# Performance work log

Measured on AMD Instinct MI355X. Metric: run time of the kernel, lower is better.

The kernel has to match this reference:

```python
import jax, jax.numpy as jnp
import numpy as np

D_MODEL = 768
NUM_HEADS = 12
HEAD_DIM = D_MODEL // NUM_HEADS


def setup_inputs() -> dict:
    key = jax.random.key(0)
    ks = jax.random.split(key, 9)
    B, S = 4, 2048
    x = jax.random.normal(ks[0], (B, S, D_MODEL), dtype=jnp.float32)
    y = jax.random.normal(ks[1], (B, S, D_MODEL), dtype=jnp.float32)
    mask = jnp.zeros((1, 1, S, S), dtype=jnp.float32)
    s = 1.0 / np.sqrt(D_MODEL)
    Wq = jax.random.normal(ks[2], (D_MODEL, D_MODEL), dtype=jnp.float32) * s
    bq = jnp.zeros((D_MODEL,), dtype=jnp.float32)
    Wkv = jax.random.normal(ks[3], (2 * D_MODEL, D_MODEL), dtype=jnp.float32) * s
    bkv = jnp.zeros((2 * D_MODEL,), dtype=jnp.float32)
    Wo = jax.random.normal(ks[4], (D_MODEL, D_MODEL), dtype=jnp.float32) * s
    bo = jnp.zeros((D_MODEL,), dtype=jnp.float32)
    return {"x": x, "y": y, "mask": mask, "Wq": Wq, "bq": bq,
            "Wkv": Wkv, "bkv": bkv, "Wo": Wo, "bo": bo}


def reference(x, y, mask, Wq, bq, Wkv, bkv, Wo, bo):
    B, S, _ = x.shape
    H, Dh = NUM_HEADS, HEAD_DIM
    # q = Linear(x); kv = Linear(y)   (torch Linear: x @ W.T + b)
    q = x @ Wq.T + bq                      # [B, S, D]
    kv = y @ Wkv.T + bkv                   # [B, S, 2D]
    q = q.reshape(B, S, H, Dh).transpose(0, 2, 1, 3)          # [B, H, S, Dh]
    kv = kv.reshape(B, S, H, 2 * Dh).transpose(0, 2, 1, 3)    # [B, H, S, 2Dh]
    k, v = kv[..., :Dh], kv[..., Dh:]
    scaled = jnp.einsum('bhqd,bhkd->bhqk', q, k) / jnp.sqrt(jnp.float32(Dh))
    scaled = scaled + mask
    attn = jax.nn.softmax(scaled, axis=-1)                    # [B, H, S, S]
    values = jnp.einsum('bhqk,bhkd->bhqd', attn, v)           # [B, H, S, Dh]
    values = values.transpose(0, 2, 1, 3).reshape(B, S, H * Dh)
    return values @ Wo.T + bo
```

## Files before the change

### kernel.cpp

```cpp
#include <hip/hip_runtime.h>
#include <cstdint>

#define S_LEN 2048
#define BATCH 4
#define NHEADS 12
#define DHEAD 64
#define DMODEL 768
#define SCALE_LOG2E 0.18033688011112042f
#define LOG2E 1.4426950408889634f

typedef unsigned short ushort_t;
typedef __attribute__((ext_vector_type(8))) __bf16 bf16x8;
typedef __attribute__((ext_vector_type(4))) float floatx4;

__device__ __forceinline__ ushort_t f2bf(float f) {
  unsigned u = __builtin_bit_cast(unsigned, f);
  u += 0x7fffu + ((u >> 16) & 1u);
  return (ushort_t)(u >> 16);
}

__device__ __forceinline__ unsigned pk2bf(float a, float b) {
  unsigned ua = __builtin_bit_cast(unsigned, a);
  unsigned ub = __builtin_bit_cast(unsigned, b);
  ua += 0x7fffu + ((ua >> 16) & 1u);
  ub += 0x7fffu + ((ub >> 16) & 1u);
  return __builtin_amdgcn_perm(ub, ua, 0x07060302);
}

__device__ __forceinline__ float fexp2(float x) {
#if __has_builtin(__builtin_amdgcn_exp2f)
  return __builtin_amdgcn_exp2f(x);
#else
  return exp2f(x);
#endif
}

__device__ __forceinline__ void gld16(const void* g, void* s) {
  __builtin_amdgcn_global_load_lds(
      (const __attribute__((address_space(1))) void*)g,
      (__attribute__((address_space(3))) void*)s, 16, 0, 0);
}

__device__ __forceinline__ floatx4 mfma16(bf16x8 a, bf16x8 b, floatx4 c) {
  return __builtin_amdgcn_mfma_f32_16x16x32_bf16(a, b, c, 0, 0, 0);
}

__global__ void init_flag(int* flag) { *flag = 1; }

__global__ void cvt_mask(const float* __restrict__ x, ushort_t* __restrict__ xb,
                         const float* __restrict__ y, ushort_t* __restrict__ yb,
                         const float* __restrict__ wq, ushort_t* __restrict__ wqb,
                         const float* __restrict__ wkv, ushort_t* __restrict__ wkvb,
                         const float* __restrict__ wo, ushort_t* __restrict__ wob,
                         const float* __restrict__ mask, int* __restrict__ flag) {
  int bx = blockIdx.x;
  if (bx >= 14592) {
    int i = (bx - 14592) * 256 + threadIdx.x;
    float4 v = ((const float4*)mask)[i];
    if (v.x != 0.f || v.y != 0.f || v.z != 0.f || v.w != 0.f) *flag = 0;
    return;
  }
  const float* s;
  ushort_t* d;
  int base;
  if (bx < 6144) { s = x; d = xb; base = bx; }
  else if (bx < 12288) { s = y; d = yb; base = bx - 6144; }
  else if (bx < 12864) { s = wq; d = wqb; base = bx - 12288; }
  else if (bx < 14016) { s = wkv; d = wkvb; base = bx - 12864; }
  else { s = wo; d = wob; base = bx - 14016; }
  int i = base * 256 + threadIdx.x;
  float4 v = ((const float4*)s)[i];
  uint2 o;
  o.x = pk2bf(v.x, v.y);
  o.y = pk2bf(v.z, v.w);
  ((uint2*)d)[i] = o;
}

#define GSTAGE(K0, BUF)                                                   \
  {                                                                       \
    gld16(ag + (K0), (char*)As + (BUF)*8192 + (wave << 10));              \
    gld16(ag + (K0) + 64 * K, (char*)As + (BUF)*8192 + (wave << 10) + 4096); \
    gld16(bg + (K0), (char*)Bs + (BUF)*8192 + (wave << 10));              \
    gld16(bg + (K0) + 64 * K, (char*)Bs + (BUF)*8192 + (wave << 10) + 4096); \
  }

__global__ __launch_bounds__(256, 3) void gemm_qkv(
    const ushort_t* __restrict__ xb, const ushort_t* __restrict__ wqb,
    const float* __restrict__ bq, ushort_t* __restrict__ Qh,
    const ushort_t* __restrict__ yb, const ushort_t* __restrict__ wkvb,
    const float* __restrict__ bkv, ushort_t* __restrict__ Kh,
    ushort_t* __restrict__ Vt) {
  __shared__ __align__(16) ushort_t As[2][128 * 32];
  __shared__ __align__(16) ushort_t Bs[2][128 * 32];
  const int tid = threadIdx.x;
  const int wave = tid >> 6, lane = tid & 63;
  const int wm = wave >> 1, wn = wave & 1;
  const bool isQ = blockIdx.x < 6;
  const int bn = (isQ ? blockIdx.x : blockIdx.x - 6) * 128;
  const int bm = blockIdx.y * 128;
  const ushort_t* A = isQ ? xb : yb;
  const ushort_t* W = isQ ? wqb : wkvb;
  const float* bias = isQ ? bq : bkv;
  const int K = DMODEL;
  const int fr = lane & 15, fq = lane >> 4;

  const int rT = tid >> 2;
  const int cT = ((tid & 3) ^ (rT & 3)) << 3;
  const ushort_t* ag = A + (size_t)(bm + rT) * K + cT;
  const ushort_t* bg = W + (size_t)(bn + rT) * K + cT;

  floatx4 acc[4][4] = {};
  GSTAGE(0, 0);
  __syncthreads();
  for (int k0 = 0; k0 < K; k0 += 32) {
    const int cur = (k0 >> 5) & 1;
    if (k0 + 32 < K) GSTAGE(k0 + 32, cur ^ 1);
    const ushort_t* Ac = As[cur];
    const ushort_t* Bc = Bs[cur];
    bf16x8 af[4], bf[4];
#pragma unroll
    for (int i = 0; i < 4; i++)
      af[i] = *(const bf16x8*)(Ac + (wm * 64 + i * 16 + fr) * 32 + ((fq ^ (fr & 3)) << 3));
#pragma unroll
    for (int j = 0; j < 4; j++)
      bf[j] = *(const bf16x8*)(Bc + (wn * 64 + j * 16 + fr) * 32 + ((fq ^ (fr & 3)) << 3));
#pragma unroll
    for (int i = 0; i < 4; i++)
#pragma unroll
      for (int j = 0; j < 4; j++)
        acc[i][j] = mfma16(af[i], bf[j], acc[i][j]);
    __syncthreads();
  }

#pragma unroll
  for (int i = 0; i < 4; i++) {
#pragma unroll
    for (int j = 0; j < 4; j++) {
#pragma unroll
      for (int r = 0; r < 4; r++) {
        int m = bm + wm * 64 + i * 16 + fq * 4 + r;
        int n = bn + wn * 64 + j * 16 + fr;
        float v = acc[i][j][r] + bias[n];
        int b = m >> 11, s = m & 2047;
        if (isQ) {
          int h = n >> 6, d = n & 63;
          Qh[(((size_t)b * NHEADS + h) * S_LEN + s) * DHEAD + d] = f2bf(v * SCALE_LOG2E);
        } else {
          int h = n >> 7, jj = n & 127;
          if (jj < 64) {
            Kh[(((size_t)b * NHEADS + h) * S_LEN + s) * DHEAD + jj] = f2bf(v);
          } else {
            int sp = (s & ~63) | ((s & 15) << 2) | ((s >> 4) & 3);
            Vt[(((size_t)b * NHEADS + h) * DHEAD + (jj - 64)) * S_LEN + sp] = f2bf(v);
          }
        }
      }
    }
  }
}

__global__ __launch_bounds__(256, 3) void gemm_out(
    const ushort_t* __restrict__ A, const ushort_t* __restrict__ W,
    const float* __restrict__ bias, float* __restrict__ o32) {
  __shared__ __align__(16) ushort_t As[2][128 * 32];
  __shared__ __align__(16) ushort_t Bs[2][128 * 32];
  const int tid = threadIdx.x;
  const int wave = tid >> 6, lane = tid & 63;
  const int wm = wave >> 1, wn = wave & 1;
  const int bm = blockIdx.y * 128, bn = blockIdx.x * 128;
  const int K = DMODEL;
  const int fr = lane & 15, fq = lane >> 4;

  const int rT = tid >> 2;
  const int cT = ((tid & 3) ^ (rT & 3)) << 3;
  const ushort_t* ag = A + (size_t)(bm + rT) * K + cT;
  const ushort_t* bg = W + (size_t)(bn + rT) * K + cT;

  floatx4 acc[4][4] = {};
  GSTAGE(0, 0);
  __syncthreads();
  for (int k0 = 0; k0 < K; k0 += 32) {
    const int cur = (k0 >> 5) & 1;
    if (k0 + 32 < K) GSTAGE(k0 + 32, cur ^ 1);
    const ushort_t* Ac = As[cur];
    const ushort_t* Bc = Bs[cur];
    bf16x8 af[4], bf[4];
#pragma unroll
    for (int i = 0; i < 4; i++)
      af[i] = *(const bf16x8*)(Ac + (wm * 64 + i * 16 + fr) * 32 + ((fq ^ (fr & 3)) << 3));
#pragma unroll
    for (int j = 0; j < 4; j++)
      bf[j] = *(const bf16x8*)(Bc + (wn * 64 + j * 16 + fr) * 32 + ((fq ^ (fr & 3)) << 3));
#pragma unroll
    for (int i = 0; i < 4; i++)
#pragma unroll
      for (int j = 0; j < 4; j++)
        acc[i][j] = mfma16(af[i], bf[j], acc[i][j]);
    __syncthreads();
  }

#pragma unroll
  for (int i = 0; i < 4; i++)
#pragma unroll
    for (int j = 0; j < 4; j++)
#pragma unroll
      for (int r = 0; r < 4; r++) {
        int m = bm + wm * 64 + i * 16 + fq * 4 + r;
        int n = bn + wn * 64 + j * 16 + fr;
        o32[(size_t)m * DMODEL + n] = acc[i][j][r] + bias[n];
      }
}

__global__ __launch_bounds__(256, 3) void flash_attn(
    const ushort_t* __restrict__ Qh, const ushort_t* __restrict__ Kh,
    const ushort_t* __restrict__ Vt, const float* __restrict__ mask,
    const int* __restrict__ mask_is_zero, ushort_t* __restrict__ Oh) {
  __shared__ __align__(16) ushort_t Ks[2][64 * 64];
  __shared__ __align__(16) ushort_t Vs[2][64 * 64];
  __shared__ __align__(16) ushort_t Ps[4][32 * 64];
  const int qt = blockIdx.x, bh = blockIdx.y;
  const int b = bh / NHEADS, h = bh % NHEADS;
  const int tid = threadIdx.x, w = tid >> 6, lane = tid & 63;
  const int li = lane & 15, lg = lane >> 4, sx = li & 7;
  const bool use_mask = (*mask_is_zero == 0);

  const int q0 = qt * 128 + w * 32;
  const ushort_t* qg = Qh + ((size_t)bh * S_LEN + q0) * DHEAD;
  bf16x8 qf[2][2];
#pragma unroll
  for (int m = 0; m < 2; m++)
#pragma unroll
    for (int kk = 0; kk < 2; kk++)
      qf[m][kk] = *(const bf16x8*)(qg + (m * 16 + li) * 64 + kk * 32 + lg * 8);

  const int srow = lane >> 3;
  const int schk = (lane & 7) ^ srow;
  const ushort_t* kg = Kh + (size_t)bh * S_LEN * DHEAD;
  const ushort_t* vg = Vt + (size_t)bh * DHEAD * S_LEN;

  float m_i[2][4], l_p[2][4];
  floatx4 o_acc[2][4] = {};
#pragma unroll
  for (int m = 0; m < 2; m++)
#pragma unroll
    for (int r = 0; r < 4; r++) { m_i[m][r] = -1e30f; l_p[m][r] = 0.f; }

#define STAGE(KT, BUF)                                                            \
  {                                                                               \
    const ushort_t* k0_ = kg + (size_t)((KT)*64 + w * 16 + srow) * 64 + schk * 8; \
    gld16(k0_, (char*)Ks + (BUF)*8192 + w * 2048);                                \
    gld16(k0_ + 8 * 64, (char*)Ks + (BUF)*8192 + w * 2048 + 1024);                \
    const ushort_t* v0_ = vg + (size_t)(w * 16 + srow) * 2048 + (KT)*64 + schk * 8; \
    gld16(v0_, (char*)Vs + (BUF)*8192 + w * 2048);                                \
    gld16(v0_ + 8 * 2048, (char*)Vs + (BUF)*8192 + w * 2048 + 1024);              \
  }

  STAGE(0, 0);
  __syncthreads();

  for (int kt = 0; kt < S_LEN / 64; kt++) {
    const int cur = kt & 1;
    if (kt < S_LEN / 64 - 1) STAGE(kt + 1, cur ^ 1);
    const ushort_t* Kc = Ks[cur];
    const ushort_t* Vc = Vs[cur];

    floatx4 sc[2][4];
#pragma unroll
    for (int c = 0; c < 4; c++) {
      bf16x8 kf0 = *(const bf16x8*)(Kc + (c * 16 + li) * 64 + ((lg ^ sx) << 3));
      bf16x8 kf1 = *(const bf16x8*)(Kc + (c * 16 + li) * 64 + (((4 + lg) ^ sx) << 3));
#pragma unroll
      for (int m = 0; m < 2; m++) {
        floatx4 s = {};
        s = mfma16(qf[m][0], kf0, s);
        s = mfma16(qf[m][1], kf1, s);
        sc[m][c] = s;
      }
    }

    if (!use_mask) {
#pragma unroll
      for (int m = 0; m < 2; m++)
#pragma unroll
        for (int r = 0; r < 4; r++) {
          float s0 = fexp2(sc[m][0][r]);
          float s1 = fexp2(sc[m][1][r]);
          float s2 = fexp2(sc[m][2][r]);
          float s3 = fexp2(sc[m][3][r]);
          sc[m][0][r] = s0; sc[m][1][r] = s1; sc[m][2][r] = s2; sc[m][3][r] = s3;
          l_p[m][r] += (s0 + s1) + (s2 + s3);
        }
    } else {
#pragma unroll
      for (int m = 0; m < 2; m++)
#pragma unroll
        for (int r = 0; r < 4; r++) {
          const float* mrow =
              mask + (size_t)(q0 + m * 16 + lg * 4 + r) * S_LEN + kt * 64;
#pragma unroll
          for (int c = 0; c < 4; c++) sc[m][c][r] += mrow[c * 16 + li] * LOG2E;
        }
      float alpha[4];
#pragma unroll
      for (int m = 0; m < 2; m++) {
#pragma unroll
        for (int r = 0; r < 4; r++) {
          float t = fmaxf(fmaxf(sc[m][0][r], sc[m][1][r]),
                          fmaxf(sc[m][2][r], sc[m][3][r]));
#pragma unroll
          for (int d = 1; d < 16; d <<= 1) t = fmaxf(t, __shfl_xor(t, d));
          float mn = fmaxf(m_i[m][r], t);
          alpha[r] = fexp2(m_i[m][r] - mn);
          m_i[m][r] = mn;
          float s0 = fexp2(sc[m][0][r] - mn);
          float s1 = fexp2(sc[m][1][r] - mn);
          float s2 = fexp2(sc[m][2][r] - mn);
          float s3 = fexp2(sc[m][3][r] - mn);
          sc[m][0][r] = s0; sc[m][1][r] = s1; sc[m][2][r] = s2; sc[m][3][r] = s3;
          l_p[m][r] = l_p[m][r] * alpha[r] + (s0 + s1) + (s2 + s3);
        }
#pragma unroll
        for (int dt = 0; dt < 4; dt++)
#pragma unroll
          for (int r = 0; r < 4; r++) o_acc[m][dt][r] *= alpha[r];
      }
    }

    ushort_t* pw = Ps[w];
#pragma unroll
    for (int m = 0; m < 2; m++)
#pragma unroll
      for (int r = 0; r < 4; r++) {
        int rho = m * 16 + lg * 4 + r;
        uint2 pv;
        pv.x = pk2bf(sc[m][0][r], sc[m][1][r]);
        pv.y = pk2bf(sc[m][2][r], sc[m][3][r]);
        *(uint2*)(pw + rho * 64 + ((((li >> 1) ^ (rho & 7)) << 3) | ((li & 1) << 2))) = pv;
      }

#pragma unroll
    for (int kk = 0; kk < 2; kk++) {
      bf16x8 pf[2];
#pragma unroll
      for (int m = 0; m < 2; m++)
        pf[m] = *(const bf16x8*)(pw + (m * 16 + li) * 64 + (((kk * 4 + lg) ^ sx) << 3));
#pragma unroll
      for (int dt = 0; dt < 4; dt++) {
        bf16x8 vf = *(const bf16x8*)(Vc + (dt * 16 + li) * 64 + (((kk * 4 + lg) ^ sx) << 3));
#pragma unroll
        for (int m = 0; m < 2; m++) o_acc[m][dt] = mfma16(pf[m], vf, o_acc[m][dt]);
      }
    }
    __syncthreads();
  }

#pragma unroll
  for (int m = 0; m < 2; m++)
#pragma unroll
    for (int r = 0; r < 4; r++) {
      float l = l_p[m][r];
#pragma unroll
      for (int d = 1; d < 16; d <<= 1) l += __shfl_xor(l, d);
      float inv = 1.0f / l;
      int row = q0 + m * 16 + lg * 4 + r;
      ushort_t* ob = Oh + ((size_t)b * S_LEN + row) * DMODEL + h * DHEAD;
#pragma unroll
      for (int dt = 0; dt < 4; dt++) ob[dt * 16 + li] = f2bf(o_acc[m][dt][r] * inv);
    }
}

extern "C" void kernel_launch(void* const* d_in, const int* in_sizes, int n_in,
                              void* d_out, int out_size, void* d_ws, size_t ws_size,
                              hipStream_t stream) {
  const float* x = (const float*)d_in[0];
  const float* y = (const float*)d_in[1];
  const float* mask = (const float*)d_in[2];
  const float* Wq = (const float*)d_in[3];
  const float* bq = (const float*)d_in[4];
  const float* Wkv = (const float*)d_in[5];
  const float* bkv = (const float*)d_in[6];
  const float* Wo = (const float*)d_in[7];
  const float* bo = (const float*)d_in[8];
  float* out = (float*)d_out;

  ushort_t* ws = (ushort_t*)d_ws;
  const size_t XN = (size_t)BATCH * S_LEN * DMODEL;
  ushort_t* xb = ws;
  ushort_t* yb = xb + XN;
  ushort_t* wqb = yb + XN;
  ushort_t* wkvb = wqb + (size_t)DMODEL * DMODEL;
  ushort_t* wob = wkvb + (size_t)2 * DMODEL * DMODEL;
  ushort_t* Qh = wob + (size_t)DMODEL * DMODEL;
  ushort_t* Kh = Qh + XN;
  ushort_t* Vt = Kh + XN;
  int* flag = (int*)(Vt + XN);
  ushort_t* Oh = xb;

  init_flag<<<1, 1, 0, stream>>>(flag);
  cvt_mask<<<18688, 256, 0, stream>>>(x, xb, y, yb, Wq, wqb, Wkv, wkvb, Wo, wob,
                                      mask, flag);
  gemm_qkv<<<dim3(18, 64), 256, 0, stream>>>(xb, wqb, bq, Qh, yb, wkvb, bkv, Kh, Vt);
  flash_attn<<<dim3(S_LEN / 128, BATCH * NHEADS), 256, 0, stream>>>(Qh, Kh, Vt, mask,
                                                                    flag, Oh);
  gemm_out<<<dim3(6, 64), 256, 0, stream>>>(Oh, wob, bo, out);
}
```

Measured before the change: 284.1 us.

## Keep attention probabilities in registers via transposed MFMA and remapped V layout

Swaps the MFMA operand order so scores come out transposed. Each lane then holds whole key strips for one query, and the bf16 P fragments can be packed directly in registers. This removes the per-wave LDS staging of P and its extra writes and reads. To match, it changes the Vt column permutation in gemm_qkv, simplifies the row max/sum reductions to two shuffles, and vectorizes the output stores. It also adds a block-index swizzle for L2 locality, uses the hardware packed bf16 convert when available, and replaces the flag-init kernel with a memset; any mismatch in the new V permutation would corrupt results.

```diff
diff --git a/kernel.cpp b/kernel.cpp
--- a/kernel.cpp
+++ b/kernel.cpp
@@ -19,6 +19,12 @@
   return (ushort_t)(u >> 16);
 }
 
+#if __has_builtin(__builtin_amdgcn_cvt_pk_bf16_f32)
+__device__ __forceinline__ unsigned pk2bf(float a, float b) {
+  auto v = __builtin_amdgcn_cvt_pk_bf16_f32(a, b);
+  return __builtin_bit_cast(unsigned, v);
+}
+#else
 __device__ __forceinline__ unsigned pk2bf(float a, float b) {
   unsigned ua = __builtin_bit_cast(unsigned, a);
   unsigned ub = __builtin_bit_cast(unsigned, b);
@@ -26,6 +32,7 @@
   ub += 0x7fffu + ((ub >> 16) & 1u);
   return __builtin_amdgcn_perm(ub, ua, 0x07060302);
 }
+#endif
 
 __device__ __forceinline__ float fexp2(float x) {
 #if __has_builtin(__builtin_amdgcn_exp2f)
@@ -44,8 +51,6 @@
 __device__ __forceinline__ floatx4 mfma16(bf16x8 a, bf16x8 b, floatx4 c) {
   return __builtin_amdgcn_mfma_f32_16x16x32_bf16(a, b, c, 0, 0, 0);
 }
-
-__global__ void init_flag(int* flag) { *flag = 1; }
 
 __global__ void cvt_mask(const float* __restrict__ x, ushort_t* __restrict__ xb,
                          const float* __restrict__ y, ushort_t* __restrict__ yb,
@@ -150,7 +155,9 @@
           if (jj < 64) {
             Kh[(((size_t)b * NHEADS + h) * S_LEN + s) * DHEAD + jj] = f2bf(v);
           } else {
-            int sp = (s & ~63) | ((s & 15) << 2) | ((s >> 4) & 3);
+            int s6 = s & 63;
+            int sp = (s & ~63) | ((s6 & 2) << 4) | (((s6 >> 2) & 3) << 3) |
+                     ((s6 & 1) << 2) | (s6 >> 4);
             Vt[(((size_t)b * NHEADS + h) * DHEAD + (jj - 64)) * S_LEN + sp] = f2bf(v);
           }
         }
@@ -217,8 +224,9 @@
     const int* __restrict__ mask_is_zero, ushort_t* __restrict__ Oh) {
   __shared__ __align__(16) ushort_t Ks[2][64 * 64];
   __shared__ __align__(16) ushort_t Vs[2][64 * 64];
-  __shared__ __align__(16) ushort_t Ps[4][32 * 64];
-  const int qt = blockIdx.x, bh = blockIdx.y;
+  const int g = blockIdx.x;
+  const int qt = (g >> 3) & 15;
+  const int bh = ((g >> 7) << 3) | (g & 7);
   const int b = bh / NHEADS, h = bh % NHEADS;
   const int tid = threadIdx.x, w = tid >> 6, lane = tid & 63;
   const int li = lane & 15, lg = lane >> 4, sx = li & 7;
@@ -238,12 +246,10 @@
   const ushort_t* kg = Kh + (size_t)bh * S_LEN * DHEAD;
   const ushort_t* vg = Vt + (size_t)bh * DHEAD * S_LEN;
 
-  float m_i[2][4], l_p[2][4];
-  floatx4 o_acc[2][4] = {};
-#pragma unroll
-  for (int m = 0; m < 2; m++)
-#pragma unroll
-    for (int r = 0; r < 4; r++) { m_i[m][r] = -1e30f; l_p[m][r] = 0.f; }
+  float m_i[2], l_pq[2];
+  floatx4 o_accT[4][2] = {};
+#pragma unroll
+  for (int m = 0; m < 2; m++) { m_i[m] = -1e30f; l_pq[m] = 0.f; }
 
 #define STAGE(KT, BUF)                                                            \
   {                                                                               \
@@ -272,101 +278,107 @@
 #pragma unroll
       for (int m = 0; m < 2; m++) {
         floatx4 s = {};
-        s = mfma16(qf[m][0], kf0, s);
-        s = mfma16(qf[m][1], kf1, s);
+        s = mfma16(kf0, qf[m][0], s);
+        s = mfma16(kf1, qf[m][1], s);
         sc[m][c] = s;
       }
     }
 
+    bf16x8 pf[2][2];
     if (!use_mask) {
 #pragma unroll
-      for (int m = 0; m < 2; m++)
-#pragma unroll
-        for (int r = 0; r < 4; r++) {
-          float s0 = fexp2(sc[m][0][r]);
-          float s1 = fexp2(sc[m][1][r]);
-          float s2 = fexp2(sc[m][2][r]);
-          float s3 = fexp2(sc[m][3][r]);
-          sc[m][0][r] = s0; sc[m][1][r] = s1; sc[m][2][r] = s2; sc[m][3][r] = s3;
-          l_p[m][r] += (s0 + s1) + (s2 + s3);
+      for (int m = 0; m < 2; m++) {
+        float cs[4];
+#pragma unroll
+        for (int c = 0; c < 4; c++) {
+          float e0 = fexp2(sc[m][c][0]);
+          float e1 = fexp2(sc[m][c][1]);
+          float e2 = fexp2(sc[m][c][2]);
+          float e3 = fexp2(sc[m][c][3]);
+          sc[m][c][0] = e0; sc[m][c][1] = e1; sc[m][c][2] = e2; sc[m][c][3] = e3;
+          cs[c] = (e0 + e1) + (e2 + e3);
         }
+        l_pq[m] += (cs[0] + cs[1]) + (cs[2] + cs[3]);
+      }
     } else {
 #pragma unroll
-      for (int m = 0; m < 2; m++)
-#pragma unroll
-        for (int r = 0; r < 4; r++) {
-          const float* mrow =
-              mask + (size_t)(q0 + m * 16 + lg * 4 + r) * S_LEN + kt * 64;
-#pragma unroll
-          for (int c = 0; c < 4; c++) sc[m][c][r] += mrow[c * 16 + li] * LOG2E;
+      for (int m = 0; m < 2; m++) {
+        int q = q0 + m * 16 + li;
+#pragma unroll
+        for (int c = 0; c < 4; c++) {
+          float4 mv = *(const float4*)(mask + (size_t)q * S_LEN + kt * 64 + c * 16 + lg * 4);
+          sc[m][c][0] += mv.x * LOG2E;
+          sc[m][c][1] += mv.y * LOG2E;
+          sc[m][c][2] += mv.z * LOG2E;
+          sc[m][c][3] += mv.w * LOG2E;
         }
-      float alpha[4];
-#pragma unroll
-      for (int m = 0; m < 2; m++) {
-#pragma unroll
-        for (int r = 0; r < 4; r++) {
-          float t = fmaxf(fmaxf(sc[m][0][r], sc[m][1][r]),
-                          fmaxf(sc[m][2][r], sc[m][3][r]));
-#pragma unroll
-          for (int d = 1; d < 16; d <<= 1) t = fmaxf(t, __shfl_xor(t, d));
-          float mn = fmaxf(m_i[m][r], t);
-          alpha[r] = fexp2(m_i[m][r] - mn);
-          m_i[m][r] = mn;
-          float s0 = fexp2(sc[m][0][r] - mn);
-          float s1 = fexp2(sc[m][1][r] - mn);
-          float s2 = fexp2(sc[m][2][r] - mn);
-          float s3 = fexp2(sc[m][3][r] - mn);
-          sc[m][0][r] = s0; sc[m][1][r] = s1; sc[m][2][r] = s2; sc[m][3][r] = s3;
-          l_p[m][r] = l_p[m][r] * alpha[r] + (s0 + s1) + (s2 + s3);
+        float mx = sc[m][0][0];
+#pragma unroll
+        for (int c = 0; c < 4; c++)
+#pragma unroll
+          for (int r = 0; r < 4; r++) mx = fmaxf(mx, sc[m][c][r]);
+        mx = fmaxf(mx, __shfl_xor(mx, 16));
+        mx = fmaxf(mx, __shfl_xor(mx, 32));
+        float mn = fmaxf(m_i[m], mx);
+        float al = fexp2(m_i[m] - mn);
+        m_i[m] = mn;
+        float cs[4];
+#pragma unroll
+        for (int c = 0; c < 4; c++) {
+          float e0 = fexp2(sc[m][c][0] - mn);
+          float e1 = fexp2(sc[m][c][1] - mn);
+          float e2 = fexp2(sc[m][c][2] - mn);
+          float e3 = fexp2(sc[m][c][3] - mn);
+          sc[m][c][0] = e0; sc[m][c][1] = e1; sc[m][c][2] = e2; sc[m][c][3] = e3;
+          cs[c] = (e0 + e1) + (e2 + e3);
         }
+        l_pq[m] = l_pq[m] * al + (cs[0] + cs[1]) + (cs[2] + cs[3]);
 #pragma unroll
         for (int dt = 0; dt < 4; dt++)
 #pragma unroll
-          for (int r = 0; r < 4; r++) o_acc[m][dt][r] *= alpha[r];
+          for (int r = 0; r < 4; r++) o_accT[dt][m][r] *= al;
       }
     }
 
-    ushort_t* pw = Ps[w];
 #pragma unroll
     for (int m = 0; m < 2; m++)
 #pragma unroll
-      for (int r = 0; r < 4; r++) {
-        int rho = m * 16 + lg * 4 + r;
-        uint2 pv;
-        pv.x = pk2bf(sc[m][0][r], sc[m][1][r]);
-        pv.y = pk2bf(sc[m][2][r], sc[m][3][r]);
-        *(uint2*)(pw + rho * 64 + ((((li >> 1) ^ (rho & 7)) << 3) | ((li & 1) << 2))) = pv;
-      }
-
-#pragma unroll
-    for (int kk = 0; kk < 2; kk++) {
-      bf16x8 pf[2];
-#pragma unroll
-      for (int m = 0; m < 2; m++)
-        pf[m] = *(const bf16x8*)(pw + (m * 16 + li) * 64 + (((kk * 4 + lg) ^ sx) << 3));
+      for (int kk = 0; kk < 2; kk++) {
+        uint4 u;
+        u.x = pk2bf(sc[m][0][2 * kk], sc[m][1][2 * kk]);
+        u.y = pk2bf(sc[m][2][2 * kk], sc[m][3][2 * kk]);
+        u.z = pk2bf(sc[m][0][2 * kk + 1], sc[m][1][2 * kk + 1]);
+        u.w = pk2bf(sc[m][2][2 * kk + 1], sc[m][3][2 * kk + 1]);
+        pf[m][kk] = __builtin_bit_cast(bf16x8, u);
+      }
+
+#pragma unroll
+    for (int kk = 0; kk < 2; kk++)
 #pragma unroll
       for (int dt = 0; dt < 4; dt++) {
         bf16x8 vf = *(const bf16x8*)(Vc + (dt * 16 + li) * 64 + (((kk * 4 + lg) ^ sx) << 3));
 #pragma unroll
-        for (int m = 0; m < 2; m++) o_acc[m][dt] = mfma16(pf[m], vf, o_acc[m][dt]);
-      }
+        for (int m = 0; m < 2; m++) o_accT[dt][m] = mfma16(vf, pf[m][kk], o_accT[dt][m]);
+      }
+    __syncthreads();
+  }
+
+#pragma unroll
+  for (int m = 0; m < 2; m++) {
+    float l = l_pq[m];
+    l += __shfl_xor(l, 16);
+    l += __shfl_xor(l, 32);
+    float inv = 1.0f / l;
+    int q = q0 + m * 16 + li;
+    ushort_t* ob = Oh + ((size_t)b * S_LEN + q) * DMODEL + h * DHEAD + lg * 4;
+#pragma unroll
+    for (int dt = 0; dt < 4; dt++) {
+      uint2 pv;
+      pv.x = pk2bf(o_accT[dt][m][0] * inv, o_accT[dt][m][1] * inv);
+      pv.y = pk2bf(o_accT[dt][m][2] * inv, o_accT[dt][m][3] * inv);
+      *(uint2*)(ob + dt * 16) = pv;
     }
-    __syncthreads();
-  }
-
-#pragma unroll
-  for (int m = 0; m < 2; m++)
-#pragma unroll
-    for (int r = 0; r < 4; r++) {
-      float l = l_p[m][r];
-#pragma unroll
-      for (int d = 1; d < 16; d <<= 1) l += __shfl_xor(l, d);
-      float inv = 1.0f / l;
-      int row = q0 + m * 16 + lg * 4 + r;
-      ushort_t* ob = Oh + ((size_t)b * S_LEN + row) * DMODEL + h * DHEAD;
-#pragma unroll
-      for (int dt = 0; dt < 4; dt++) ob[dt * 16 + li] = f2bf(o_acc[m][dt][r] * inv);
-    }
+  }
 }
 
 extern "C" void kernel_launch(void* const* d_in, const int* in_sizes, int n_in,
@@ -396,11 +408,10 @@
   int* flag = (int*)(Vt + XN);
   ushort_t* Oh = xb;
 
-  init_flag<<<1, 1, 0, stream>>>(flag);
+  hipMemsetAsync(flag, 1, 4, stream);
   cvt_mask<<<18688, 256, 0, stream>>>(x, xb, y, yb, Wq, wqb, Wkv, wkvb, Wo, wob,
                                       mask, flag);
   gemm_qkv<<<dim3(18, 64), 256, 0, stream>>>(xb, wqb, bq, Qh, yb, wkvb, bkv, Kh, Vt);
-  flash_attn<<<dim3(S_LEN / 128, BATCH * NHEADS), 256, 0, stream>>>(Qh, Kh, Vt, mask,
-                                                                    flag, Oh);
+  flash_attn<<<768, 256, 0, stream>>>(Qh, Kh, Vt, mask, flag, Oh);
   gemm_out<<<dim3(6, 64), 256, 0, stream>>>(Oh, wob, bo, out);
 }
```

Result: faster. 270.8 us (-4.7%).
